# Optimization experiments

Measured on AMD Instinct MI355X. Metric: run time of the kernel, lower is better.

The kernel has to match this reference:

```python
import jax, jax.numpy as jnp
import numpy as np
import math

N_HEAD = 8
LN_EPS = 1e-5


def _layernorm(x, w, b):
    # Biased variance as in the triton kernel: var = E[x^2] - mean^2
    mean = jnp.mean(x, axis=-1, keepdims=True)
    var = jnp.mean(x * x, axis=-1, keepdims=True) - mean * mean
    return (x - mean) * jax.lax.rsqrt(var + LN_EPS) * w + b


def _gelu_tanh(x):
    # matches triton gelu: tanh approximation
    return 0.5 * x * (1.0 + jnp.tanh(0.7978845608 * (x + 0.044715 * x * x * x)))


def _causal_attention(qkv, n_head):
    B, T, C3 = qkv.shape
    C = C3 // 3
    D = C // n_head
    q, k, v = jnp.split(qkv, 3, axis=-1)
    q = q.reshape(B, T, n_head, D)
    k = k.reshape(B, T, n_head, D)
    v = v.reshape(B, T, n_head, D)
    scale = 1.0 / math.sqrt(D)
    scores = jnp.einsum('bqhd,bkhd->bhqk', q, k) * scale  # [B,H,T,T]
    causal = jnp.tril(jnp.ones((T, T), dtype=bool))
    scores = jnp.where(causal, scores, -jnp.inf)
    p = jax.nn.softmax(scores, axis=-1)
    out = jnp.einsum('bhqk,bkhd->bqhd', p, v)
    return out.reshape(B, T, C)


def setup_inputs() -> dict:
    key = jax.random.key(0)
    ks = jax.random.split(key, 8)
    B, T, C = 8, 2048, 768
    s = 0.02
    return {
        'x': jax.random.normal(ks[0], (B, T, C), jnp.float32),
        'ln1_w': jnp.ones((C,), jnp.float32),
        'ln1_b': jnp.zeros((C,), jnp.float32),
        'w_qkv': jax.random.normal(ks[1], (3 * C, C), jnp.float32) * s,
        'b_qkv': jnp.zeros((3 * C,), jnp.float32),
        'w_attn_proj': jax.random.normal(ks[2], (C, C), jnp.float32) * s,
        'b_attn_proj': jnp.zeros((C,), jnp.float32),
        'ln2_w': jnp.ones((C,), jnp.float32),
        'ln2_b': jnp.zeros((C,), jnp.float32),
        'w_fc': jax.random.normal(ks[3], (4 * C, C), jnp.float32) * s,
        'b_fc': jnp.zeros((4 * C,), jnp.float32),
        'w_mlp_proj': jax.random.normal(ks[4], (C, 4 * C), jnp.float32) * s,
        'b_mlp_proj': jnp.zeros((C,), jnp.float32),
    }


def reference(x, ln1_w, ln1_b, w_qkv, b_qkv, w_attn_proj, b_attn_proj,
              ln2_w, ln2_b, w_fc, b_fc, w_mlp_proj, b_mlp_proj):
    # attention block: fused LN + QKV linear, causal flash attention, out proj, residual
    qkv = _layernorm(x, ln1_w, ln1_b) @ w_qkv.T + b_qkv          # [B,T,3C]
    att = _causal_attention(qkv, N_HEAD)                          # [B,T,C]
    x = x + (att @ w_attn_proj.T + b_attn_proj)
    # MLP block: fused LN + fc + gelu, proj, residual
    h = _gelu_tanh(_layernorm(x, ln2_w, ln2_b) @ w_fc.T + b_fc)   # [B,T,4C]
    x = x + (h @ w_mlp_proj.T + b_mlp_proj)
    return x
```

## Files before the change

kernel.cpp:

```cpp
#include <hip/hip_runtime.h>
#include <hip/hip_bf16.h>
#include <cstdint>
#include <cstddef>

typedef __attribute__((ext_vector_type(8))) short bf16x8;
typedef __attribute__((ext_vector_type(4))) short bf16x4;
typedef __attribute__((ext_vector_type(4))) float f32x4;
typedef __attribute__((ext_vector_type(16))) float f32x16;

#define GLB_AS(p) ((const __attribute__((address_space(1))) void*)(p))
#define LDS_AS(p) ((__attribute__((address_space(3))) void*)(p))

__device__ __forceinline__ short f2bf(float f) {
    union { float f; unsigned u; } x; x.f = f;
    unsigned r = (x.u + 0x7fffu + ((x.u >> 16) & 1u)) >> 16;
    return (short)r;
}
__device__ __forceinline__ unsigned packbf2(float a, float b) {
    union { float f; unsigned u; } x, y; x.f = a; y.f = b;
    return (x.u >> 16) | (y.u & 0xffff0000u);
}
__device__ __forceinline__ f32x4 MF(bf16x8 a, bf16x8 b, f32x4 c) {
    return __builtin_amdgcn_mfma_f32_16x16x32_bf16(a, b, c, 0, 0, 0);
}
__device__ __forceinline__ f32x16 MF32(bf16x8 a, bf16x8 b, f32x16 c) {
    return __builtin_amdgcn_mfma_f32_32x32x16_bf16(a, b, c, 0, 0, 0);
}

__global__ __launch_bounds__(256) void k_cast_bf16(const float* __restrict__ src,
                                                   short* __restrict__ dst, int n4) {
    int i = blockIdx.x * 256 + threadIdx.x;
    int stride = gridDim.x * 256;
    for (; i < n4; i += stride) {
        float4 v = ((const float4*)src)[i];
        bf16x4 o;
        o[0] = f2bf(v.x); o[1] = f2bf(v.y); o[2] = f2bf(v.z); o[3] = f2bf(v.w);
        ((bf16x4*)dst)[i] = o;
    }
}

__global__ __launch_bounds__(256) void k_layernorm(const float* __restrict__ x,
                                                   const float* __restrict__ w,
                                                   const float* __restrict__ b,
                                                   short* __restrict__ out) {
    const int row = blockIdx.x;
    const int tid = threadIdx.x;
    const float* xr = x + (size_t)row * 768;
    float v0 = xr[tid], v1 = xr[tid + 256], v2 = xr[tid + 512];
    float s = v0 + v1 + v2;
    float ss = v0 * v0 + v1 * v1 + v2 * v2;
    #pragma unroll
    for (int m = 32; m; m >>= 1) { s += __shfl_xor(s, m); ss += __shfl_xor(ss, m); }
    __shared__ float red[8];
    int wid = tid >> 6, lane = tid & 63;
    if (lane == 0) { red[wid] = s; red[4 + wid] = ss; }
    __syncthreads();
    s = red[0] + red[1] + red[2] + red[3];
    ss = red[4] + red[5] + red[6] + red[7];
    float mean = s * (1.f / 768.f);
    float var = ss * (1.f / 768.f) - mean * mean;
    float inv = rsqrtf(var + 1e-5f);
    short* orow = out + (size_t)row * 768;
    orow[tid]       = f2bf((v0 - mean) * inv * w[tid]       + b[tid]);
    orow[tid + 256] = f2bf((v1 - mean) * inv * w[tid + 256] + b[tid + 256]);
    orow[tid + 512] = f2bf((v2 - mean) * inv * w[tid + 512] + b[tid + 512]);
}

#define QUAD(MB, NB, AA, BB)                                                   \
    do {                                                                       \
        __builtin_amdgcn_s_setprio(1);                                         \
        _Pragma("unroll")                                                      \
        for (int mi = 0; mi < 4; ++mi)                                         \
            _Pragma("unroll")                                                  \
            for (int ni = 0; ni < 2; ++ni) {                                   \
                acc[(MB) + mi][(NB) + ni] =                                    \
                    MF(AA[mi][0], BB[ni][0], acc[(MB) + mi][(NB) + ni]);       \
                acc[(MB) + mi][(NB) + ni] =                                    \
                    MF(AA[mi][1], BB[ni][1], acc[(MB) + mi][(NB) + ni]);       \
            }                                                                  \
        __builtin_amdgcn_s_setprio(0);                                         \
    } while (0)

template <int EPI>
__global__ __launch_bounds__(512, 2) void k_gemm256(const short* __restrict__ A,
                                                    const short* __restrict__ B,
                                                    const float* __restrict__ bias,
                                                    const float* __restrict__ res,
                                                    void* __restrict__ out,
                                                    int M, int N, int K) {
    __shared__ short As[2][256 * 64];
    __shared__ short Bs[2][256 * 64];
    const int tid = threadIdx.x, lane = tid & 63, wid = tid >> 6;
    const int l4 = lane & 15, lh = lane >> 4;
    const int wm = wid >> 2, wn = wid & 3;
    const int gx = gridDim.x;
    const int nwg = gx * gridDim.y;
    int wg = blockIdx.y * gx + blockIdx.x;
    { const int q = nwg >> 3; wg = (wg & 7) * q + (wg >> 3); }
    const int row0 = (wg / gx) * 256, col0 = (wg % gx) * 256;

    auto stage = [&](const short* __restrict__ src, int base_row, short* lds,
                     int mh, int k0) {
        #pragma unroll
        for (int i = 0; i < 2; ++i) {
            const int chunk = wid * 2 + i;
            const int dl = mh * 16384 + chunk * 1024 + lane * 16;
            const int r = dl >> 7;
            const int cb = (dl & 127) ^ ((r & 7) << 4);
            __builtin_amdgcn_global_load_lds(
                GLB_AS(src + (size_t)(base_row + r) * K + k0 + (cb >> 1)),
                LDS_AS(lds + mh * 8192 + chunk * 512), 16, 0, 0);
        }
    };
    auto rd = [&](const short* lds, int r, int kb) -> bf16x8 {
        return *(const bf16x8*)((const char*)lds + r * 128 +
                                ((kb * 64 + lh * 16) ^ ((r & 7) << 4)));
    };

    f32x4 acc[8][4] = {};
    bf16x8 a[4][2], b0[2][2], b1[2][2];
    const int NT = K >> 6;

    stage(A, row0, As[0], 0, 0);
    stage(A, row0, As[0], 1, 0);
    stage(B, col0, Bs[0], 0, 0);
    stage(B, col0, Bs[0], 1, 0);
    asm volatile("s_waitcnt vmcnt(0)" ::: "memory");
    __builtin_amdgcn_s_barrier();

    for (int t = 0; t < NT - 1; ++t) {
        const int cur = t & 1, nxt = cur ^ 1;
        const short* Ac = As[cur];
        const short* Bc = Bs[cur];
        const int kn = (t + 1) << 6;
        #pragma unroll
        for (int mi = 0; mi < 4; ++mi) {
            const int r = wm * 128 + mi * 16 + l4;
            a[mi][0] = rd(Ac, r, 0); a[mi][1] = rd(Ac, r, 1);
        }
        #pragma unroll
        for (int ni = 0; ni < 2; ++ni) {
            const int r = wn * 64 + ni * 16 + l4;
            b0[ni][0] = rd(Bc, r, 0); b0[ni][1] = rd(Bc, r, 1);
        }
        stage(A, row0, As[nxt], 0, kn);
        stage(A, row0, As[nxt], 1, kn);
        QUAD(0, 0, a, b0);
        __builtin_amdgcn_s_barrier();
        #pragma unroll
        for (int ni = 0; ni < 2; ++ni) {
            const int r = wn * 64 + (2 + ni) * 16 + l4;
            b1[ni][0] = rd(Bc, r, 0); b1[ni][1] = rd(Bc, r, 1);
        }
        stage(B, col0, Bs[nxt], 0, kn);
        stage(B, col0, Bs[nxt], 1, kn);
        QUAD(0, 2, a, b1);
        __builtin_amdgcn_s_barrier();
        #pragma unroll
        for (int mi = 0; mi < 4; ++mi) {
            const int r = wm * 128 + (4 + mi) * 16 + l4;
            a[mi][0] = rd(Ac, r, 0); a[mi][1] = rd(Ac, r, 1);
        }
        QUAD(4, 2, a, b1);
        __builtin_amdgcn_s_barrier();
        QUAD(4, 0, a, b0);
        asm volatile("s_waitcnt vmcnt(0)" ::: "memory");
        __builtin_amdgcn_s_barrier();
    }
    {
        const int cur = (NT - 1) & 1;
        const short* Ac = As[cur];
        const short* Bc = Bs[cur];
        #pragma unroll
        for (int mi = 0; mi < 4; ++mi) {
            const int r = wm * 128 + mi * 16 + l4;
            a[mi][0] = rd(Ac, r, 0); a[mi][1] = rd(Ac, r, 1);
        }
        #pragma unroll
        for (int ni = 0; ni < 2; ++ni) {
            const int r = wn * 64 + ni * 16 + l4;
            b0[ni][0] = rd(Bc, r, 0); b0[ni][1] = rd(Bc, r, 1);
        }
        QUAD(0, 0, a, b0);
        #pragma unroll
        for (int ni = 0; ni < 2; ++ni) {
            const int r = wn * 64 + (2 + ni) * 16 + l4;
            b1[ni][0] = rd(Bc, r, 0); b1[ni][1] = rd(Bc, r, 1);
        }
        QUAD(0, 2, a, b1);
        #pragma unroll
        for (int mi = 0; mi < 4; ++mi) {
            const int r = wm * 128 + (4 + mi) * 16 + l4;
            a[mi][0] = rd(Ac, r, 0); a[mi][1] = rd(Ac, r, 1);
        }
        QUAD(4, 2, a, b1);
        QUAD(4, 0, a, b0);
    }

    #pragma unroll
    for (int mi = 0; mi < 8; ++mi) {
        const int rowb = row0 + wm * 128 + mi * 16 + lh * 4;
        #pragma unroll
        for (int ni = 0; ni < 4; ++ni) {
            const int col = col0 + wn * 64 + ni * 16 + l4;
            const float bv = bias[col];
            #pragma unroll
            for (int j = 0; j < 4; ++j) {
                const size_t idx = (size_t)(rowb + j) * N + col;
                float v = acc[mi][ni][j] + bv;
                if (EPI == 0) {
                    ((short*)out)[idx] = f2bf(v);
                } else if (EPI == 1) {
                    ((float*)out)[idx] = v + res[idx];
                } else {
                    float u = v + 0.044715f * v * v * v;
                    float t = 1.f - 2.f / (__expf(1.5957691216f * u) + 1.f);
                    ((short*)out)[idx] = f2bf(0.5f * v * (1.f + t));
                }
            }
        }
    }
}

__global__ __launch_bounds__(256, 2) void k_attn6(const short* __restrict__ qkv,
                                                  short* __restrict__ att) {
    __shared__ short Ks[2][64 * 128];
    __shared__ short Vs[2][96 * 64];
    const int tid = threadIdx.x, lane = tid & 63, wid = tid >> 6;
    const int lq = lane & 31, hi = lane >> 5;
    const int h = blockIdx.y, b = blockIdx.z;
    const short* base = qkv + (size_t)b * 2048 * 2304 + h * 96;
    const short* Kb = base + 768;
    const short* Vb = base + 1536;
    const int vkvr = (tid / 12) * 4, vd0 = (tid % 12) * 8;
    const int vslot = (vkvr & ~12) | ((vkvr & 4) << 1) | ((vkvr & 8) >> 1);
    bf16x8 vreg[4];
    const float QSC = 0.14724445f;

    auto stageK = [&](int jt, int bb) {
        const int kv0 = jt * 64;
        for (int c = wid; c < 16; c += 4) {
            const int dl = c * 1024 + lane * 16;
            const int row = dl >> 8;
            const int scol = (dl & 255) ^ ((row & 7) << 4);
            __builtin_amdgcn_global_load_lds(GLB_AS(Kb + (size_t)(kv0 + row) * 2304 + (scol >> 1)),
                                             LDS_AS(&Ks[bb][c * 512]), 16, 0, 0);
        }
    };
    auto loadV = [&](int jt) {
        if (tid < 192) {
            const int kv0 = jt * 64;
            #pragma unroll
            for (int e = 0; e < 4; ++e)
                vreg[e] = *(const bf16x8*)(Vb + (size_t)(kv0 + vkvr + e) * 2304 + vd0);
        }
    };
    auto writeV = [&](int bb) {
        if (tid < 192) {
            #pragma unroll
            for (int f = 0; f < 8; ++f) {
                const int row = vd0 + f;
                const int sw = ((row & 7) ^ ((row >> 3) & 7)) << 4;
                const int byte = (row * 128 + vslot * 2) ^ sw;
                bf16x4 w4;
                w4[0] = vreg[0][f]; w4[1] = vreg[1][f]; w4[2] = vreg[2][f]; w4[3] = vreg[3][f];
                *(bf16x4*)((char*)&Vs[bb][0] + byte) = w4;
            }
        }
    };

    for (int half = 0; half < 2; ++half) {
        const int qt = half ? 15 - (int)blockIdx.x : (int)blockIdx.x;
        const int q0 = qt * 128 + wid * 32;
        const int qa = q0 + lq;

        bf16x8 qf[6];
        #pragma unroll
        for (int kb = 0; kb < 6; ++kb) {
            bf16x8 v = *(const bf16x8*)(base + (size_t)qa * 2304 + kb * 16 + hi * 8);
            #pragma unroll
            for (int e = 0; e < 8; ++e) {
                union { unsigned u; float f; } x;
                x.u = ((unsigned)(unsigned short)v[e]) << 16;
                qf[kb][e] = f2bf(x.f * QSC);
            }
        }

        f32x16 o[3] = {};
        float lrow = 0.f;
        const int nt = 2 * qt + 2;

        stageK(0, 0);
        loadV(0);
        asm volatile("s_waitcnt vmcnt(0)" ::: "memory");
        writeV(0);
        __syncthreads();

        int cur = 0;
        for (int jt = 0; jt < nt; ++jt) {
            const int nxt = cur ^ 1;
            const bool more = (jt + 1 < nt);
            if (more) { stageK(jt + 1, nxt); loadV(jt + 1); }

            const int kv0 = jt * 64;
            if (kv0 <= q0 + 31) {
                const bool full = (kv0 + 63 <= q0);
                f32x16 s0 = {}, s1 = {};
                #pragma unroll
                for (int kb = 0; kb < 6; ++kb) {
                    const int r0 = lq, r1 = 32 + lq;
                    bf16x8 kf0 = *(const bf16x8*)((const char*)&Ks[cur][0] +
                                  r0 * 256 + ((kb * 32 + hi * 16) ^ ((r0 & 7) << 4)));
                    bf16x8 kf1 = *(const bf16x8*)((const char*)&Ks[cur][0] +
                                  r1 * 256 + ((kb * 32 + hi * 16) ^ ((r1 & 7) << 4)));
                    s0 = MF32(kf0, qf[kb], s0);
                    s1 = MF32(kf1, qf[kb], s1);
                }
                if (!full) {
                    #pragma unroll
                    for (int r = 0; r < 16; ++r) {
                        const int kvl = (r & 3) + 8 * (r >> 2) + 4 * hi;
                        if (kv0 + kvl > qa) s0[r] = -INFINITY;
                        if (kv0 + 32 + kvl > qa) s1[r] = -INFINITY;
                    }
                }
                #pragma unroll
                for (int r = 0; r < 16; ++r) {
                    s0[r] = exp2f(s0[r]);
                    s1[r] = exp2f(s1[r]);
                }
                float ar[16];
                #pragma unroll
                for (int r = 0; r < 16; ++r) ar[r] = s0[r] + s1[r];
                #pragma unroll
                for (int st = 8; st; st >>= 1)
                    #pragma unroll
                    for (int r = 0; r < 8; ++r)
                        if (r < st) ar[r] += ar[r + st];
                lrow += ar[0] + __shfl_xor(ar[0], 32);
                unsigned pk0[8], pk1[8];
                #pragma unroll
                for (int j = 0; j < 8; ++j) {
                    pk0[j] = packbf2(s0[2 * j], s0[2 * j + 1]);
                    pk1[j] = packbf2(s1[2 * j], s1[2 * j + 1]);
                }
                #pragma unroll
                for (int db = 0; db < 3; ++db) {
                    const int vrow = db * 32 + lq;
                    const int vsw = ((vrow & 7) ^ ((vrow >> 3) & 7)) << 4;
                    #pragma unroll
                    for (int c = 0; c < 4; ++c) {
                        bf16x8 vf = *(const bf16x8*)((const char*)&Vs[cur][0] +
                                     vrow * 128 + ((c * 32 + hi * 16) ^ vsw));
                        union { unsigned u[4]; bf16x8 v; } pa;
                        const unsigned* pk = (c < 2) ? pk0 : pk1;
                        const int o4 = (c & 1) * 4;
                        pa.u[0] = pk[o4]; pa.u[1] = pk[o4 + 1];
                        pa.u[2] = pk[o4 + 2]; pa.u[3] = pk[o4 + 3];
                        o[db] = MF32(vf, pa.v, o[db]);
                    }
                }
            }

            if (more) {
                asm volatile("s_waitcnt vmcnt(0)" ::: "memory");
                writeV(nxt);
            }
            __syncthreads();
            cur = nxt;
        }

        const float inv = 1.f / lrow;
        short* orow = att + (size_t)((size_t)b * 2048 + qa) * 768 + h * 96;
        #pragma unroll
        for (int db = 0; db < 3; ++db)
            #pragma unroll
            for (int j = 0; j < 4; ++j) {
                bf16x4 ov;
                #pragma unroll
                for (int e = 0; e < 4; ++e) ov[e] = f2bf(o[db][4 * j + e] * inv);
                *(bf16x4*)(orow + db * 32 + 8 * j + 4 * hi) = ov;
            }
    }
}

extern "C" void kernel_launch(void* const* d_in, const int* in_sizes, int n_in,
                              void* d_out, int out_size, void* d_ws, size_t ws_size,
                              hipStream_t stream) {
    (void)in_sizes; (void)n_in; (void)out_size; (void)ws_size;
    const float* x      = (const float*)d_in[0];
    const float* ln1_w  = (const float*)d_in[1];
    const float* ln1_b  = (const float*)d_in[2];
    const float* w_qkv  = (const float*)d_in[3];
    const float* b_qkv  = (const float*)d_in[4];
    const float* w_proj = (const float*)d_in[5];
    const float* b_proj = (const float*)d_in[6];
    const float* ln2_w  = (const float*)d_in[7];
    const float* ln2_b  = (const float*)d_in[8];
    const float* w_fc   = (const float*)d_in[9];
    const float* b_fc   = (const float*)d_in[10];
    const float* w_mlp  = (const float*)d_in[11];
    const float* b_mlp  = (const float*)d_in[12];

    const int C = 768, M = 8 * 2048;

    char* ws = (char*)d_ws;
    size_t off = 0;
    auto alloc = [&](size_t bytes) {
        char* p = ws + off;
        off += (bytes + 255) & ~(size_t)255;
        return p;
    };
    short* wqkv_b = (short*)alloc((size_t)3 * C * C * 2);
    short* wproj_b = (short*)alloc((size_t)C * C * 2);
    short* wfc_b  = (short*)alloc((size_t)4 * C * C * 2);
    short* wmlp_b = (short*)alloc((size_t)4 * C * C * 2);
    short* bufA   = (short*)alloc((size_t)M * C * 2);
    short* bufB   = (short*)alloc((size_t)M * 4 * C * 2);
    float* x2     = (float*)alloc((size_t)M * C * 4);

    k_cast_bf16<<<dim3(432), dim3(256), 0, stream>>>(w_qkv, wqkv_b, 3 * C * C / 4);
    k_cast_bf16<<<dim3(144), dim3(256), 0, stream>>>(w_proj, wproj_b, C * C / 4);
    k_cast_bf16<<<dim3(576), dim3(256), 0, stream>>>(w_fc, wfc_b, 4 * C * C / 4);
    k_cast_bf16<<<dim3(576), dim3(256), 0, stream>>>(w_mlp, wmlp_b, 4 * C * C / 4);

    k_layernorm<<<dim3(M), dim3(256), 0, stream>>>(x, ln1_w, ln1_b, bufA);
    k_gemm256<0><<<dim3(2304 / 256, M / 256), dim3(512), 0, stream>>>(
        bufA, wqkv_b, b_qkv, nullptr, bufB, M, 2304, C);
    k_attn6<<<dim3(8, 8, 8), dim3(256), 0, stream>>>(bufB, bufA);
    k_gemm256<1><<<dim3(C / 256, M / 256), dim3(512), 0, stream>>>(
        bufA, wproj_b, b_proj, x, x2, M, C, C);
    k_layernorm<<<dim3(M), dim3(256), 0, stream>>>(x2, ln2_w, ln2_b, bufA);
    k_gemm256<2><<<dim3(3072 / 256, M / 256), dim3(512), 0, stream>>>(
        bufA, wfc_b, b_fc, nullptr, bufB, M, 3072, C);
    k_gemm256<1><<<dim3(C / 256, M / 256), dim3(512), 0, stream>>>(
        bufB, wmlp_b, b_mlp, x2, d_out, M, C, 4 * C);
}
```

Before: 447.3 us.

## Triple-buffer A tiles in GEMM to prefetch two K-steps ahead

The bf16 GEMM kernel now keeps three LDS buffers for the A operand and two for B. A tiles are prefetched two K iterations ahead and B tiles one ahead, and the loop waits with vmcnt(4) so the newest A loads can stay in flight across the barrier. The separate peeled last iteration is folded into the loop with guarded staging. This aims to hide global-load latency behind MFMA work, at the cost of raising LDS use to 160KB per block and adding branches in the loop.

```diff
diff --git a/kernel.cpp b/kernel.cpp
--- a/kernel.cpp
+++ b/kernel.cpp
@@ -88,8 +88,8 @@
                                                     const float* __restrict__ res,
                                                     void* __restrict__ out,
                                                     int M, int N, int K) {
-    __shared__ short As[2][256 * 64];
-    __shared__ short Bs[2][256 * 64];
+    __shared__ short As3[3][256 * 64];
+    __shared__ short Bs2[2][256 * 64];
     const int tid = threadIdx.x, lane = tid & 63, wid = tid >> 6;
     const int l4 = lane & 15, lh = lane >> 4;
     const int wm = wid >> 2, wn = wid & 3;
@@ -121,18 +121,17 @@
     bf16x8 a[4][2], b0[2][2], b1[2][2];
     const int NT = K >> 6;
 
-    stage(A, row0, As[0], 0, 0);
-    stage(A, row0, As[0], 1, 0);
-    stage(B, col0, Bs[0], 0, 0);
-    stage(B, col0, Bs[0], 1, 0);
-    asm volatile("s_waitcnt vmcnt(0)" ::: "memory");
+    stage(A, row0, As3[0], 0, 0);  stage(A, row0, As3[0], 1, 0);
+    stage(B, col0, Bs2[0], 0, 0);  stage(B, col0, Bs2[0], 1, 0);
+    stage(A, row0, As3[1], 0, 64); stage(A, row0, As3[1], 1, 64);
+    asm volatile("s_waitcnt vmcnt(4)" ::: "memory");
     __builtin_amdgcn_s_barrier();
 
-    for (int t = 0; t < NT - 1; ++t) {
-        const int cur = t & 1, nxt = cur ^ 1;
-        const short* Ac = As[cur];
-        const short* Bc = Bs[cur];
-        const int kn = (t + 1) << 6;
+    int ia = 0, ia2 = 2, ib = 0;
+    for (int t = 0; t < NT; ++t) {
+        const short* Ac = As3[ia];
+        const short* Bc = Bs2[ib];
+        const int ib2 = ib ^ 1;
         #pragma unroll
         for (int mi = 0; mi < 4; ++mi) {
             const int r = wm * 128 + mi * 16 + l4;
@@ -143,8 +142,16 @@
             const int r = wn * 64 + ni * 16 + l4;
             b0[ni][0] = rd(Bc, r, 0); b0[ni][1] = rd(Bc, r, 1);
         }
-        stage(A, row0, As[nxt], 0, kn);
-        stage(A, row0, As[nxt], 1, kn);
+        if (t + 1 < NT) {
+            const int kn = (t + 1) << 6;
+            stage(B, col0, Bs2[ib2], 0, kn);
+            stage(B, col0, Bs2[ib2], 1, kn);
+        }
+        if (t + 2 < NT) {
+            const int kn2 = (t + 2) << 6;
+            stage(A, row0, As3[ia2], 0, kn2);
+            stage(A, row0, As3[ia2], 1, kn2);
+        }
         QUAD(0, 0, a, b0);
         __builtin_amdgcn_s_barrier();
         #pragma unroll
@@ -152,8 +159,6 @@
             const int r = wn * 64 + (2 + ni) * 16 + l4;
             b1[ni][0] = rd(Bc, r, 0); b1[ni][1] = rd(Bc, r, 1);
         }
-        stage(B, col0, Bs[nxt], 0, kn);
-        stage(B, col0, Bs[nxt], 1, kn);
         QUAD(0, 2, a, b1);
         __builtin_amdgcn_s_barrier();
         #pragma unroll
@@ -164,37 +169,15 @@
         QUAD(4, 2, a, b1);
         __builtin_amdgcn_s_barrier();
         QUAD(4, 0, a, b0);
-        asm volatile("s_waitcnt vmcnt(0)" ::: "memory");
+        if (t + 2 < NT) {
+            asm volatile("s_waitcnt vmcnt(4)" ::: "memory");
+        } else if (t + 1 < NT) {
+            asm volatile("s_waitcnt vmcnt(0)" ::: "memory");
+        }
         __builtin_amdgcn_s_barrier();
-    }
-    {
-        const int cur = (NT - 1) & 1;
-        const short* Ac = As[cur];
-        const short* Bc = Bs[cur];
-        #pragma unroll
-        for (int mi = 0; mi < 4; ++mi) {
-            const int r = wm * 128 + mi * 16 + l4;
-            a[mi][0] = rd(Ac, r, 0); a[mi][1] = rd(Ac, r, 1);
-        }
-        #pragma unroll
-        for (int ni = 0; ni < 2; ++ni) {
-            const int r = wn * 64 + ni * 16 + l4;
-            b0[ni][0] = rd(Bc, r, 0); b0[ni][1] = rd(Bc, r, 1);
-        }
-        QUAD(0, 0, a, b0);
-        #pragma unroll
-        for (int ni = 0; ni < 2; ++ni) {
-            const int r = wn * 64 + (2 + ni) * 16 + l4;
-            b1[ni][0] = rd(Bc, r, 0); b1[ni][1] = rd(Bc, r, 1);
-        }
-        QUAD(0, 2, a, b1);
-        #pragma unroll
-        for (int mi = 0; mi < 4; ++mi) {
-            const int r = wm * 128 + (4 + mi) * 16 + l4;
-            a[mi][0] = rd(Ac, r, 0); a[mi][1] = rd(Ac, r, 1);
-        }
-        QUAD(4, 2, a, b1);
-        QUAD(4, 0, a, b0);
+        ia = (ia + 1 == 3) ? 0 : ia + 1;
+        ia2 = (ia2 + 1 == 3) ? 0 : ia2 + 1;
+        ib = ib2;
     }
 
     #pragma unroll
```

New measurement: 478.0 us. 1.07x slower.
